# Kernel tuning notes

Hardware: AMD Instinct MI355X
Metric: run time of the kernel (lower is better)

The kernel has to match this reference:

```python
import jax, jax.numpy as jnp
import numpy as np


def setup_inputs() -> dict:
    key0 = jax.random.key(0)
    ks = jax.random.split(key0, 9)
    B, S, D, A = 32, 2048, 1024, 1024
    query = jax.random.normal(ks[0], (B, D), dtype=jnp.float32)
    key = jax.random.normal(ks[1], (B, S, D), dtype=jnp.float32)
    value = jax.random.normal(ks[2], (B, S, D), dtype=jnp.float32)
    # Dense params (glorot-ish scale)
    Wq = jax.random.normal(ks[3], (D, A), dtype=jnp.float32) * (1.0 / np.sqrt(D))
    bq = jnp.zeros((A,), dtype=jnp.float32)
    Wk = jax.random.normal(ks[4], (D, A), dtype=jnp.float32) * (1.0 / np.sqrt(D))
    bk = jnp.zeros((A,), dtype=jnp.float32)
    Wa = jax.random.normal(ks[5], (A, 1), dtype=jnp.float32) * (1.0 / np.sqrt(A))
    ba = jnp.zeros((1,), dtype=jnp.float32)
    return {"query": query, "key": key, "value": value,
            "Wq": Wq, "bq": bq, "Wk": Wk, "bk": bk, "Wa": Wa, "ba": ba}


def reference(query, key, value, Wq, bq, Wk, bk, Wa, ba):
    # query: [B, D] -> [B, 1, A]
    query_proj = (query @ Wq + bq)[:, None, :]
    # key: [B, S, D] -> [B, S, A]
    key_proj = jnp.einsum('bsd,da->bsa', key, Wk) + bk
    act = jnp.tanh(query_proj + key_proj)            # [B, S, A]
    att_proj = jnp.einsum('bsa,ao->bso', act, Wa) + ba  # [B, S, 1]
    att_weights = jax.nn.softmax(att_proj, axis=1)   # softmax over seq dim
    # weighted sum over seq: [B, 1, D]
    context_vector = jnp.sum(att_weights * value, axis=1, keepdims=True)
    return context_vector, att_weights
```

## Files before the change

kernel.cpp:

```cpp
#include <hip/hip_runtime.h>
#include <hip/hip_bf16.h>

typedef _Float16 f16x8 __attribute__((ext_vector_type(8)));
typedef _Float16 f16x4 __attribute__((ext_vector_type(4)));
typedef float f32x4 __attribute__((ext_vector_type(4)));

#define SD 1024
#define SEQ 2048
#define NB 32
#define M_TOTAL (NB * SEQ)
#define BM 64
#define LDS_KEY_BYTES (BM * SD * 2)
#define LDS_TOTAL (LDS_KEY_BYTES + 8*64*4)

__device__ __forceinline__ float tanh_fast(float x) {
  float e = __expf(2.0f * x);
  return 1.0f - 2.0f / (e + 1.0f);
}

__global__ void k_qproj(const float* __restrict__ query, const float* __restrict__ Wq,
                        const float* __restrict__ bq, const float* __restrict__ bk,
                        float* __restrict__ qpb) {
  const int a = blockIdx.x * 256 + threadIdx.x;
  const int b = blockIdx.y;
  const float* q = query + b * SD;
  float s = 0.f;
#pragma unroll 8
  for (int d = 0; d < SD; ++d) s = fmaf(q[d], Wq[d * SD + a], s);
  qpb[b * SD + a] = s + bq[a] + bk[a];
}

__global__ void k_packWk(const float* __restrict__ Wk, _Float16* __restrict__ WkB) {
  const int idx = blockIdx.x * 256 + threadIdx.x;
  const int k = idx >> 10, n = idx & 1023;
  const int nt = n >> 4, kk = k >> 5;
  const int l = (((k >> 3) & 3) << 4) | (n & 15);
  const int j = k & 7;
  WkB[((((nt << 5) + kk) << 6) + l) * 8 + j] = (_Float16)Wk[idx];
}

__global__ __launch_bounds__(512, 2) void k_main(
    const float* __restrict__ key, const _Float16* __restrict__ WkB,
    const float* __restrict__ qpb, const float* __restrict__ Wa,
    float* __restrict__ logits) {
  extern __shared__ char lds[];
  float* red = (float*)(lds + LDS_KEY_BYTES);
  const int tid = threadIdx.x;
  const int wave = tid >> 6;
  const int lane = tid & 63;
  const int m0 = blockIdx.x * BM;
  const int b = m0 >> 11;

  {
    const float4* kp = (const float4*)(key + (size_t)m0 * SD);
#pragma unroll 4
    for (int i = 0; i < 32; ++i) {
      const int idx = i * 512 + tid;
      const float4 v = kp[idx];
      const int row = idx >> 8;
      const int c4 = idx & 255;
      f16x4 h;
      h[0] = (_Float16)v.x; h[1] = (_Float16)v.y;
      h[2] = (_Float16)v.z; h[3] = (_Float16)v.w;
      const int off = (row * 2048 + c4 * 8) ^ ((row & 7) << 4);
      *(f16x4*)(lds + off) = h;
    }
  }
  __syncthreads();

  const int lane15 = lane & 15;
  const int lq = lane >> 4;
  const int swz = (lane15 & 7) << 4;
  int abase[4];
#pragma unroll
  for (int mt = 0; mt < 4; ++mt)
    abase[mt] = (mt * 16 + lane15) * 2048 + lq * 16;

  const f16x8* WkB8 = (const f16x8*)WkB;
  const float* qpb_b = qpb + b * SD;

  float lp[16];
#pragma unroll
  for (int i = 0; i < 16; ++i) lp[i] = 0.f;

  for (int g = 0; g < 2; ++g) {
    const int ng0 = wave * 128 + g * 64;
    const int ntg0 = ng0 >> 4;
    f32x4 acc[4][4];
#pragma unroll
    for (int mt = 0; mt < 4; ++mt)
#pragma unroll
      for (int nt = 0; nt < 4; ++nt)
        acc[mt][nt] = (f32x4){0.f, 0.f, 0.f, 0.f};

    f16x8 af[2][4], bf[2][4];
#pragma unroll
    for (int mt = 0; mt < 4; ++mt)
      af[0][mt] = *(const f16x8*)(lds + ((abase[mt] + 0) ^ swz));
#pragma unroll
    for (int nt = 0; nt < 4; ++nt)
      bf[0][nt] = WkB8[(ntg0 + nt) * 2048 + lane];

#pragma unroll 2
    for (int kk = 0; kk < 32; ++kk) {
      const int cur = kk & 1, nxt = cur ^ 1;
      if (kk < 31) {
#pragma unroll
        for (int mt = 0; mt < 4; ++mt)
          af[nxt][mt] = *(const f16x8*)(lds + ((abase[mt] + (kk + 1) * 64) ^ swz));
#pragma unroll
        for (int nt = 0; nt < 4; ++nt)
          bf[nxt][nt] = WkB8[(ntg0 + nt) * 2048 + (kk + 1) * 64 + lane];
      }
#pragma unroll
      for (int mt = 0; mt < 4; ++mt)
#pragma unroll
        for (int nt = 0; nt < 4; ++nt)
          acc[mt][nt] = __builtin_amdgcn_mfma_f32_16x16x32_f16(
              af[cur][mt], bf[cur][nt], acc[mt][nt], 0, 0, 0);
    }

#pragma unroll
    for (int nt = 0; nt < 4; ++nt) {
      const int col = ng0 + nt * 16 + lane15;
      const float qv = qpb_b[col];
      const float wv = Wa[col];
#pragma unroll
      for (int mt = 0; mt < 4; ++mt)
#pragma unroll
        for (int j = 0; j < 4; ++j) {
          const float t = tanh_fast(acc[mt][nt][j] + qv);
          lp[mt * 4 + j] = fmaf(t, wv, lp[mt * 4 + j]);
        }
    }
  }

#pragma unroll
  for (int i = 0; i < 16; ++i) {
    float v = lp[i];
    v += __shfl_xor(v, 1, 16);
    v += __shfl_xor(v, 2, 16);
    v += __shfl_xor(v, 4, 16);
    v += __shfl_xor(v, 8, 16);
    lp[i] = v;
  }
  if (lane15 == 0) {
#pragma unroll
    for (int mt = 0; mt < 4; ++mt)
#pragma unroll
      for (int j = 0; j < 4; ++j)
        red[wave * 64 + mt * 16 + lq * 4 + j] = lp[mt * 4 + j];
  }
  __syncthreads();
  if (tid < BM) {
    float s = 0.f;
#pragma unroll
    for (int w = 0; w < 8; ++w) s += red[w * 64 + tid];
    logits[m0 + tid] = s;
  }
}

__global__ void k_softmax(float* __restrict__ att) {
  const int b = blockIdx.x, t = threadIdx.x;
  __shared__ float red[4];
  float* row = att + b * SEQ;
  float v[8];
  float mx = -3.0e38f;
#pragma unroll
  for (int i = 0; i < 8; ++i) { v[i] = row[i * 256 + t]; mx = fmaxf(mx, v[i]); }
#pragma unroll
  for (int m = 1; m < 64; m <<= 1) mx = fmaxf(mx, __shfl_xor(mx, m, 64));
  if ((t & 63) == 0) red[t >> 6] = mx;
  __syncthreads();
  mx = fmaxf(fmaxf(red[0], red[1]), fmaxf(red[2], red[3]));
  __syncthreads();
  float s = 0.f;
#pragma unroll
  for (int i = 0; i < 8; ++i) { v[i] = __expf(v[i] - mx); s += v[i]; }
#pragma unroll
  for (int m = 1; m < 64; m <<= 1) s += __shfl_xor(s, m, 64);
  if ((t & 63) == 0) red[t >> 6] = s;
  __syncthreads();
  s = red[0] + red[1] + red[2] + red[3];
  const float inv = 1.0f / s;
#pragma unroll
  for (int i = 0; i < 8; ++i) row[i * 256 + t] = v[i] * inv;
}

__global__ void k_ctx(const float* __restrict__ value, const float* __restrict__ att,
                      float4* __restrict__ partials) {
  const int bx = blockIdx.x;
  const int b = bx >> 4, sl = bx & 15;
  const int t = threadIdx.x;
  const float4* vp = (const float4*)(value + (size_t)(b * SEQ + sl * 128) * SD);
  const float* ap = att + b * SEQ + sl * 128;
  float4 acc = make_float4(0.f, 0.f, 0.f, 0.f);
#pragma unroll 4
  for (int s = 0; s < 128; ++s) {
    const float w = ap[s];
    const float4 v = vp[s * 256 + t];
    acc.x = fmaf(w, v.x, acc.x); acc.y = fmaf(w, v.y, acc.y);
    acc.z = fmaf(w, v.z, acc.z); acc.w = fmaf(w, v.w, acc.w);
  }
  partials[(b * 16 + sl) * 256 + t] = acc;
}

__global__ void k_fin(const float* __restrict__ partials, float* __restrict__ ctx) {
  const int i = blockIdx.x * 256 + threadIdx.x;
  const int b = i >> 10, d = i & 1023;
  float s = 0.f;
#pragma unroll
  for (int sl = 0; sl < 16; ++sl) s += partials[(b * 16 + sl) * SD + d];
  ctx[i] = s;
}

extern "C" void kernel_launch(void* const* d_in, const int* in_sizes, int n_in,
                              void* d_out, int out_size, void* d_ws, size_t ws_size,
                              hipStream_t stream) {
  const float* query = (const float*)d_in[0];
  const float* key   = (const float*)d_in[1];
  const float* value = (const float*)d_in[2];
  const float* Wq    = (const float*)d_in[3];
  const float* bq    = (const float*)d_in[4];
  const float* Wk    = (const float*)d_in[5];
  const float* bk    = (const float*)d_in[6];
  const float* Wa    = (const float*)d_in[7];

  float* out = (float*)d_out;
  float* ctx_out = out;
  float* att_out = out + NB * SD;

  char* ws = (char*)d_ws;
  float* qpb = (float*)ws;
  _Float16* WkB = (_Float16*)(ws + 131072);
  float* partials = (float*)(ws + 131072);

  hipFuncSetAttribute(reinterpret_cast<const void*>(k_main),
                      hipFuncAttributeMaxDynamicSharedMemorySize, LDS_TOTAL);

  k_qproj<<<dim3(4, NB), 256, 0, stream>>>(query, Wq, bq, bk, qpb);
  k_packWk<<<4096, 256, 0, stream>>>(Wk, WkB);
  k_main<<<M_TOTAL / BM, 512, LDS_TOTAL, stream>>>(key, WkB, qpb, Wa, att_out);
  k_softmax<<<NB, 256, 0, stream>>>(att_out);
  k_ctx<<<NB * 16, 256, 0, stream>>>(value, att_out, (float4*)partials);
  k_fin<<<NB * SD / 256, 256, 0, stream>>>(partials, ctx_out);
}
```

Baseline: 306.3 us.

## Make k_main persistent with register-staged prefetch of next key chunk

The main GEMM kernel now launches 256 persistent blocks that each loop over 4 row chunks of 64 instead of 1024 one-shot blocks. The next chunk's fp32 key tile is loaded into registers while the current chunk's tanh epilogue and reduction run, so global key loads overlap compute. The B-fragment prefetch is also deepened to two iterations ahead with a 4-slot ring. The cost is 128 extra VGPRs for staging, which could cause spills or lower occupancy under launch_bounds(512,2), and fewer blocks are available to balance load across CUs.

```diff
diff --git a/kernel.cpp b/kernel.cpp
--- a/kernel.cpp
+++ b/kernel.cpp
@@ -10,6 +10,8 @@
 #define NB 32
 #define M_TOTAL (NB * SEQ)
 #define BM 64
+#define NBLK 256
+#define CHUNKS (M_TOTAL / BM / NBLK)
 #define LDS_KEY_BYTES (BM * SD * 2)
 #define LDS_TOTAL (LDS_KEY_BYTES + 8*64*4)
 
@@ -48,115 +50,147 @@
   const int tid = threadIdx.x;
   const int wave = tid >> 6;
   const int lane = tid & 63;
-  const int m0 = blockIdx.x * BM;
-  const int b = m0 >> 11;
-
+  const int lane15 = lane & 15;
+  const int lq = lane >> 4;
+  const int swz = (lane15 & 7) << 4;
+
+  const int row0 = blockIdx.x * (BM * CHUNKS);
+  const int b = row0 >> 11;
+  const float* qpb_b = qpb + b * SD;
+  const f16x8* WkB8 = (const f16x8*)WkB;
+
+  int abase[4];
+#pragma unroll
+  for (int mt = 0; mt < 4; ++mt)
+    abase[mt] = (mt * 16 + lane15) * 2048 + lq * 16;
+
+  float4 stg[32];
   {
-    const float4* kp = (const float4*)(key + (size_t)m0 * SD);
-#pragma unroll 4
+    const float4* kp = (const float4*)(key + (size_t)row0 * SD);
+#pragma unroll
+    for (int i = 0; i < 32; ++i) stg[i] = kp[i * 512 + tid];
+  }
+
+  for (int c = 0; c < CHUNKS; ++c) {
+    const int m0 = row0 + c * BM;
+
+#pragma unroll
     for (int i = 0; i < 32; ++i) {
       const int idx = i * 512 + tid;
-      const float4 v = kp[idx];
       const int row = idx >> 8;
       const int c4 = idx & 255;
       f16x4 h;
-      h[0] = (_Float16)v.x; h[1] = (_Float16)v.y;
-      h[2] = (_Float16)v.z; h[3] = (_Float16)v.w;
-      const int off = (row * 2048 + c4 * 8) ^ ((row & 7) << 4);
-      *(f16x4*)(lds + off) = h;
-    }
-  }
-  __syncthreads();
-
-  const int lane15 = lane & 15;
-  const int lq = lane >> 4;
-  const int swz = (lane15 & 7) << 4;
-  int abase[4];
-#pragma unroll
-  for (int mt = 0; mt < 4; ++mt)
-    abase[mt] = (mt * 16 + lane15) * 2048 + lq * 16;
-
-  const f16x8* WkB8 = (const f16x8*)WkB;
-  const float* qpb_b = qpb + b * SD;
-
-  float lp[16];
-#pragma unroll
-  for (int i = 0; i < 16; ++i) lp[i] = 0.f;
-
-  for (int g = 0; g < 2; ++g) {
-    const int ng0 = wave * 128 + g * 64;
-    const int ntg0 = ng0 >> 4;
-    f32x4 acc[4][4];
-#pragma unroll
-    for (int mt = 0; mt < 4; ++mt)
+      h[0] = (_Float16)stg[i].x; h[1] = (_Float16)stg[i].y;
+      h[2] = (_Float16)stg[i].z; h[3] = (_Float16)stg[i].w;
+      *(f16x4*)(lds + ((row * 2048 + c4 * 8) ^ ((row & 7) << 4))) = h;
+    }
+    __syncthreads();
+
+    float lp[16];
+#pragma unroll
+    for (int i = 0; i < 16; ++i) lp[i] = 0.f;
+
+    for (int g = 0; g < 2; ++g) {
+      const int ng0 = wave * 128 + g * 64;
+      const int ntg0 = ng0 >> 4;
+
+      f32x4 acc[4][4];
+#pragma unroll
+      for (int mt = 0; mt < 4; ++mt)
+#pragma unroll
+        for (int nt = 0; nt < 4; ++nt)
+          acc[mt][nt] = (f32x4){0.f, 0.f, 0.f, 0.f};
+
+      f16x8 af[2][4], bf[4][4];
+#pragma unroll
+      for (int mt = 0; mt < 4; ++mt)
+        af[0][mt] = *(const f16x8*)(lds + ((abase[mt]) ^ swz));
 #pragma unroll
       for (int nt = 0; nt < 4; ++nt)
-        acc[mt][nt] = (f32x4){0.f, 0.f, 0.f, 0.f};
-
-    f16x8 af[2][4], bf[2][4];
-#pragma unroll
-    for (int mt = 0; mt < 4; ++mt)
-      af[0][mt] = *(const f16x8*)(lds + ((abase[mt] + 0) ^ swz));
-#pragma unroll
-    for (int nt = 0; nt < 4; ++nt)
-      bf[0][nt] = WkB8[(ntg0 + nt) * 2048 + lane];
-
-#pragma unroll 2
-    for (int kk = 0; kk < 32; ++kk) {
-      const int cur = kk & 1, nxt = cur ^ 1;
-      if (kk < 31) {
-#pragma unroll
-        for (int mt = 0; mt < 4; ++mt)
-          af[nxt][mt] = *(const f16x8*)(lds + ((abase[mt] + (kk + 1) * 64) ^ swz));
+        bf[0][nt] = WkB8[(ntg0 + nt) * 2048 + lane];
+#pragma unroll
+      for (int nt = 0; nt < 4; ++nt)
+        bf[1][nt] = WkB8[(ntg0 + nt) * 2048 + 64 + lane];
+
+#pragma unroll 4
+      for (int kk = 0; kk < 28; ++kk) {
 #pragma unroll
         for (int nt = 0; nt < 4; ++nt)
-          bf[nxt][nt] = WkB8[(ntg0 + nt) * 2048 + (kk + 1) * 64 + lane];
+          bf[(kk + 2) & 3][nt] = WkB8[(ntg0 + nt) * 2048 + (kk + 2) * 64 + lane];
+#pragma unroll
+        for (int mt = 0; mt < 4; ++mt)
+          af[(kk + 1) & 1][mt] = *(const f16x8*)(lds + ((abase[mt] + (kk + 1) * 64) ^ swz));
+#pragma unroll
+        for (int mt = 0; mt < 4; ++mt)
+#pragma unroll
+          for (int nt = 0; nt < 4; ++nt)
+            acc[mt][nt] = __builtin_amdgcn_mfma_f32_16x16x32_f16(
+                af[kk & 1][mt], bf[kk & 3][nt], acc[mt][nt], 0, 0, 0);
       }
 #pragma unroll
+      for (int kk = 28; kk < 32; ++kk) {
+        if (kk < 30) {
+#pragma unroll
+          for (int nt = 0; nt < 4; ++nt)
+            bf[(kk + 2) & 3][nt] = WkB8[(ntg0 + nt) * 2048 + (kk + 2) * 64 + lane];
+        }
+        if (kk < 31) {
+#pragma unroll
+          for (int mt = 0; mt < 4; ++mt)
+            af[(kk + 1) & 1][mt] = *(const f16x8*)(lds + ((abase[mt] + (kk + 1) * 64) ^ swz));
+        }
+#pragma unroll
+        for (int mt = 0; mt < 4; ++mt)
+#pragma unroll
+          for (int nt = 0; nt < 4; ++nt)
+            acc[mt][nt] = __builtin_amdgcn_mfma_f32_16x16x32_f16(
+                af[kk & 1][mt], bf[kk & 3][nt], acc[mt][nt], 0, 0, 0);
+      }
+
+#pragma unroll
+      for (int nt = 0; nt < 4; ++nt) {
+        const int col = ng0 + nt * 16 + lane15;
+        const float qv = qpb_b[col];
+        const float wv = Wa[col];
+#pragma unroll
+        for (int mt = 0; mt < 4; ++mt)
+#pragma unroll
+          for (int j = 0; j < 4; ++j) {
+            const float t = tanh_fast(acc[mt][nt][j] + qv);
+            lp[mt * 4 + j] = fmaf(t, wv, lp[mt * 4 + j]);
+          }
+      }
+    }
+
+    if (c + 1 < CHUNKS) {
+      const float4* kp = (const float4*)(key + (size_t)(m0 + BM) * SD);
+#pragma unroll
+      for (int i = 0; i < 32; ++i) stg[i] = kp[i * 512 + tid];
+    }
+
+#pragma unroll
+    for (int i = 0; i < 16; ++i) {
+      float v = lp[i];
+      v += __shfl_xor(v, 1, 16);
+      v += __shfl_xor(v, 2, 16);
+      v += __shfl_xor(v, 4, 16);
+      v += __shfl_xor(v, 8, 16);
+      lp[i] = v;
+    }
+    if (lane15 == 0) {
+#pragma unroll
       for (int mt = 0; mt < 4; ++mt)
 #pragma unroll
-        for (int nt = 0; nt < 4; ++nt)
-          acc[mt][nt] = __builtin_amdgcn_mfma_f32_16x16x32_f16(
-              af[cur][mt], bf[cur][nt], acc[mt][nt], 0, 0, 0);
-    }
-
-#pragma unroll
-    for (int nt = 0; nt < 4; ++nt) {
-      const int col = ng0 + nt * 16 + lane15;
-      const float qv = qpb_b[col];
-      const float wv = Wa[col];
-#pragma unroll
-      for (int mt = 0; mt < 4; ++mt)
-#pragma unroll
-        for (int j = 0; j < 4; ++j) {
-          const float t = tanh_fast(acc[mt][nt][j] + qv);
-          lp[mt * 4 + j] = fmaf(t, wv, lp[mt * 4 + j]);
-        }
-    }
-  }
-
-#pragma unroll
-  for (int i = 0; i < 16; ++i) {
-    float v = lp[i];
-    v += __shfl_xor(v, 1, 16);
-    v += __shfl_xor(v, 2, 16);
-    v += __shfl_xor(v, 4, 16);
-    v += __shfl_xor(v, 8, 16);
-    lp[i] = v;
-  }
-  if (lane15 == 0) {
-#pragma unroll
-    for (int mt = 0; mt < 4; ++mt)
-#pragma unroll
-      for (int j = 0; j < 4; ++j)
-        red[wave * 64 + mt * 16 + lq * 4 + j] = lp[mt * 4 + j];
-  }
-  __syncthreads();
-  if (tid < BM) {
-    float s = 0.f;
-#pragma unroll
-    for (int w = 0; w < 8; ++w) s += red[w * 64 + tid];
-    logits[m0 + tid] = s;
+        for (int j = 0; j < 4; ++j)
+          red[wave * 64 + mt * 16 + lq * 4 + j] = lp[mt * 4 + j];
+    }
+    __syncthreads();
+    if (tid < BM) {
+      float s = 0.f;
+#pragma unroll
+      for (int w = 0; w < 8; ++w) s += red[w * 64 + tid];
+      logits[m0 + tid] = s;
+    }
   }
 }
 
@@ -240,7 +274,7 @@
 
   k_qproj<<<dim3(4, NB), 256, 0, stream>>>(query, Wq, bq, bk, qpb);
   k_packWk<<<4096, 256, 0, stream>>>(Wk, WkB);
-  k_main<<<M_TOTAL / BM, 512, LDS_TOTAL, stream>>>(key, WkB, qpb, Wa, att_out);
+  k_main<<<NBLK, 512, LDS_TOTAL, stream>>>(key, WkB, qpb, Wa, att_out);
   k_softmax<<<NB, 256, 0, stream>>>(att_out);
   k_ctx<<<NB * 16, 256, 0, stream>>>(value, att_out, (float4*)partials);
   k_fin<<<NB * SD / 256, 256, 0, stream>>>(partials, ctx_out);
```

After: 446.6 us. 1.46x slower.
